# Kernel optimization log

Hardware: AMD Instinct MI355X
Metric: run time of the kernel (lower is better)

## Reference

```python
import jax, jax.numpy as jnp
import numpy as np

N = 50000       # n_points
E = 1000000     # number of events
P = 200000      # node_pair_samples
S = 50          # riemann_samples
EPS = 1e-6      # torch PairwiseDistance eps added to the difference
NON_EVENT_W = 1.0


def setup_inputs() -> dict:
    key = jax.random.key(0)
    ks = jax.random.split(key, 8)
    unif = lambda k, shp: (jax.random.uniform(k, shp) * 0.05 - 0.025).astype(jnp.float32)
    return {
        "beta": jnp.full((1, 1), 1.0, dtype=jnp.float32),
        "z0": unif(ks[0], (N, 2)),
        "v0": unif(ks[1], (N, 2)),
        "a0": unif(ks[2], (N, 2)),
        "events_t": (jax.random.uniform(ks[3], (E,)) * 10.0).astype(jnp.float32),
        "events_uv": jax.random.randint(ks[4], (E, 2), 0, N, dtype=jnp.int32),
        "pairs_u": jax.random.randint(ks[5], (P,), 0, N, dtype=jnp.int32),
        "pairs_v": jax.random.randint(ks[6], (P,), 0, N, dtype=jnp.int32),
        "t0": 0,
        "tn": 10,
    }


def reference(beta, z0, v0, a0, events_t, events_uv, pairs_u, pairs_v, t0, tn):
    # ---- event intensity: sum_e (beta - ||z_u(t_e) - z_v(t_e)||) ----
    u = events_uv[:, 0]
    v = events_uv[:, 1]
    t = events_t[:, None]                          # (E,1)
    # z(t) = z0 + v0*t + 0.5*a0*t^2; only the pair difference is needed
    diff = (z0[u] - z0[v]) + (v0[u] - v0[v]) * t + 0.5 * (a0[u] - a0[v]) * t * t + EPS  # (E,2)
    d = jnp.sqrt(jnp.sum(diff * diff, axis=-1))    # (E,)
    n_events = jnp.asarray(d.shape[0], dtype=beta.dtype)
    event_intensity = n_events * beta - jnp.sum(d)  # (1,1)

    # ---- non-event intensity: Riemann midpoint sum of exp(beta - dist) ----
    t0f = jnp.asarray(t0, dtype=jnp.float32)
    tnf = jnp.asarray(tn, dtype=jnp.float32)
    dx = (tnf - t0f) / S
    t_mid = t0f + (jnp.arange(S, dtype=jnp.float32) + 0.5) * dx  # (S,) midpoints of linspace
    dz = (z0[pairs_u] - z0[pairs_v])[:, None, :]   # (P,1,2)
    dv = (v0[pairs_u] - v0[pairs_v])[:, None, :]
    da = (a0[pairs_u] - a0[pairs_v])[:, None, :]
    tm = t_mid[None, :, None]                      # (1,S,1)
    diffp = dz + dv * tm + 0.5 * da * tm * tm + EPS  # (P,S,2)
    dp = jnp.sqrt(jnp.sum(diffp * diffp, axis=-1))   # (P,S)
    non_event_intensity = jnp.sum(jnp.exp(beta[0, 0] - dp)) * dx

    return event_intensity - NON_EVENT_W * non_event_intensity  # (1,1)
```

## Files before the change

### kernel.cpp

```cpp
#include <hip/hip_runtime.h>
#include <hip/hip_fp16.h>

#define N_NODES 50000
#define E_COUNT 1000000
#define HALF_E  (E_COUNT / 2)
#define P_COUNT 200000
#define S_COUNT 50
#define EPS_F   1e-6f

constexpr int TPB = 256;
constexpr int EVENT_BLOCKS = (HALF_E + TPB - 1) / TPB;
constexpr int PAIR_BLOCKS  = (P_COUNT + TPB - 1) / TPB;
constexpr int TOTAL_BLOCKS = EVENT_BLOCKS + PAIR_BLOCKS;

__device__ __forceinline__ float block_reduce_sum(float v) {
    #pragma unroll
    for (int m = 32; m >= 1; m >>= 1) v += __shfl_xor(v, m, 64);
    __shared__ float smem[TPB / 64];
    const int lane = threadIdx.x & 63;
    const int wid  = threadIdx.x >> 6;
    if (lane == 0) smem[wid] = v;
    __syncthreads();
    float r = 0.0f;
    if (threadIdx.x == 0) {
        #pragma unroll
        for (int w = 0; w < TPB / 64; ++w) r += smem[w];
    }
    __syncthreads();
    return r;
}

__global__ __launch_bounds__(TPB) void pack_nodes_kernel(
    const float2* __restrict__ z0,
    const float2* __restrict__ v0,
    const float2* __restrict__ a0,
    float4*       __restrict__ packed)
{
    const int i = blockIdx.x * TPB + threadIdx.x;
    if (i < N_NODES) {
        const float2 z = z0[i], v = v0[i], a = a0[i];
        float4 r;
        r.x = z.x;
        r.y = z.y;
        r.z = __builtin_bit_cast(float, __floats2half2_rn(v.x, v.y));
        r.w = __builtin_bit_cast(float, __floats2half2_rn(a.x, a.y));
        packed[i] = r;
    }
}

__device__ __forceinline__ float event_dist(const float4 pu, const float4 pv,
                                            const float t) {
    const float2 vu = __half22float2(__builtin_bit_cast(__half2, pu.z));
    const float2 vv = __half22float2(__builtin_bit_cast(__half2, pv.z));
    const float2 au = __half22float2(__builtin_bit_cast(__half2, pu.w));
    const float2 av = __half22float2(__builtin_bit_cast(__half2, pv.w));
    const float ht2 = 0.5f * t * t;
    const float fx = (pu.x - pv.x) + (vu.x - vv.x) * t + (au.x - av.x) * ht2 + EPS_F;
    const float fy = (pu.y - pv.y) + (vu.y - vv.y) * t + (au.y - av.y) * ht2 + EPS_F;
    return sqrtf(fx * fx + fy * fy);
}

__global__ __launch_bounds__(TPB) void fused_partials_kernel(
    const float4* __restrict__ packed,
    const float*  __restrict__ events_t,
    const int*    __restrict__ events_uv_flat,
    const int*    __restrict__ pairs_u,
    const int*    __restrict__ pairs_v,
    const int*    __restrict__ t0p,
    const int*    __restrict__ tnp,
    float*        __restrict__ partials)
{
    float acc = 0.0f;
    const int b = blockIdx.x;

    if (b < PAIR_BLOCKS) {
        const int i = b * TPB + threadIdx.x;
        if (i < P_COUNT) {
            const float t0f = (float)t0p[0];
            const float tnf = (float)tnp[0];
            const float dxs = (tnf - t0f) / (float)S_COUNT;
            const int u = __builtin_nontemporal_load(pairs_u + i);
            const int v = __builtin_nontemporal_load(pairs_v + i);
            const float4 pu = packed[u];
            const float4 pv = packed[v];
            const float2 vu = __half22float2(__builtin_bit_cast(__half2, pu.z));
            const float2 vv = __half22float2(__builtin_bit_cast(__half2, pv.z));
            const float2 au = __half22float2(__builtin_bit_cast(__half2, pu.w));
            const float2 av = __half22float2(__builtin_bit_cast(__half2, pv.w));
            const float dzx = pu.x - pv.x,          dzy = pu.y - pv.y;
            const float dvx = vu.x - vv.x,          dvy = vu.y - vv.y;
            const float dax = 0.5f * (au.x - av.x), day = 0.5f * (au.y - av.y);
            float sacc = 0.0f;
            #pragma unroll 5
            for (int s = 0; s < S_COUNT; ++s) {
                const float tm = t0f + ((float)s + 0.5f) * dxs;
                const float fx = dzx + dvx * tm + dax * tm * tm + EPS_F;
                const float fy = dzy + dvy * tm + day * tm * tm + EPS_F;
                const float dp = sqrtf(fx * fx + fy * fy);
                sacc += __expf(-dp);
            }
            acc = sacc;
        }
    } else {
        const int gid = (b - PAIR_BLOCKS) * TPB + threadIdx.x;
        if (gid < HALF_E) {
            const float t0 = __builtin_nontemporal_load(events_t + gid);
            const float t1 = __builtin_nontemporal_load(events_t + gid + HALF_E);
            const int u0 = __builtin_nontemporal_load(events_uv_flat + 2 * gid);
            const int w0 = __builtin_nontemporal_load(events_uv_flat + 2 * gid + 1);
            const int u1 = __builtin_nontemporal_load(events_uv_flat + 2 * (gid + HALF_E));
            const int w1 = __builtin_nontemporal_load(events_uv_flat + 2 * (gid + HALF_E) + 1);
            const float4 p0u = packed[u0];
            const float4 p0v = packed[w0];
            const float4 p1u = packed[u1];
            const float4 p1v = packed[w1];
            acc = event_dist(p0u, p0v, t0) + event_dist(p1u, p1v, t1);
        }
    }

    const float r = block_reduce_sum(acc);
    if (threadIdx.x == 0) partials[b] = r;
}

__global__ __launch_bounds__(TPB) void finalize_kernel(
    const float* __restrict__ partials,
    const float* __restrict__ beta,
    const int*   __restrict__ t0p,
    const int*   __restrict__ tnp,
    float*       __restrict__ out)
{
    float accP = 0.0f, accE = 0.0f;
    for (int i = threadIdx.x; i < PAIR_BLOCKS; i += TPB) accP += partials[i];
    for (int i = PAIR_BLOCKS + threadIdx.x; i < TOTAL_BLOCKS; i += TPB) accE += partials[i];

    const float sumExp = block_reduce_sum(accP);
    const float sumD   = block_reduce_sum(accE);

    if (threadIdx.x == 0) {
        const float bta = beta[0];
        const float t0f = (float)t0p[0];
        const float tnf = (float)tnp[0];
        const float dxs = (tnf - t0f) / (float)S_COUNT;
        const float event_intensity     = (float)E_COUNT * bta - sumD;
        const float non_event_intensity = expf(bta) * sumExp * dxs;
        out[0] = event_intensity - non_event_intensity;
    }
}

extern "C" void kernel_launch(void* const* d_in, const int* in_sizes, int n_in,
                              void* d_out, int out_size, void* d_ws, size_t ws_size,
                              hipStream_t stream) {
    const float*  beta      = (const float*)d_in[0];
    const float2* z0        = (const float2*)d_in[1];
    const float2* v0        = (const float2*)d_in[2];
    const float2* a0        = (const float2*)d_in[3];
    const float*  events_t  = (const float*)d_in[4];
    const int*    events_uv = (const int*)d_in[5];
    const int*    pairs_u   = (const int*)d_in[6];
    const int*    pairs_v   = (const int*)d_in[7];
    const int*    t0p       = (const int*)d_in[8];
    const int*    tnp       = (const int*)d_in[9];

    const size_t packed_off = 16384;
    float* partials = (float*)d_ws;
    float4* packed  = (float4*)((char*)d_ws + packed_off);
    float* out      = (float*)d_out;

    pack_nodes_kernel<<<(N_NODES + TPB - 1) / TPB, TPB, 0, stream>>>(z0, v0, a0, packed);

    fused_partials_kernel<<<TOTAL_BLOCKS, TPB, 0, stream>>>(
        packed, events_t, events_uv, pairs_u, pairs_v, t0p, tnp, partials);

    finalize_kernel<<<1, TPB, 0, stream>>>(partials, beta, t0p, tnp, out);
}
```

Baseline: 28.44 us.

## Fuse final reduction into main kernel via last-block atomic counter; 4 events per thread

```diff
diff --git a/kernel.cpp b/kernel.cpp
--- a/kernel.cpp
+++ b/kernel.cpp
@@ -3,15 +3,16 @@
 
 #define N_NODES 50000
 #define E_COUNT 1000000
-#define HALF_E  (E_COUNT / 2)
 #define P_COUNT 200000
 #define S_COUNT 50
 #define EPS_F   1e-6f
 
 constexpr int TPB = 256;
-constexpr int EVENT_BLOCKS = (HALF_E + TPB - 1) / TPB;
+constexpr int EPT = 4;
+constexpr int EQ  = E_COUNT / EPT;
+constexpr int EVENT_BLOCKS = (EQ + TPB - 1) / TPB;
 constexpr int PAIR_BLOCKS  = (P_COUNT + TPB - 1) / TPB;
-constexpr int TOTAL_BLOCKS = EVENT_BLOCKS + PAIR_BLOCKS;
+constexpr int TOTAL_BLOCKS = PAIR_BLOCKS + EVENT_BLOCKS;
 
 __device__ __forceinline__ float block_reduce_sum(float v) {
     #pragma unroll
@@ -34,9 +35,11 @@
     const float2* __restrict__ z0,
     const float2* __restrict__ v0,
     const float2* __restrict__ a0,
-    float4*       __restrict__ packed)
+    float4*       __restrict__ packed,
+    unsigned*     __restrict__ counter)
 {
     const int i = blockIdx.x * TPB + threadIdx.x;
+    if (i == 0) *counter = 0u;
     if (i < N_NODES) {
         const float2 z = z0[i], v = v0[i], a = a0[i];
         float4 r;
@@ -60,15 +63,18 @@
     return sqrtf(fx * fx + fy * fy);
 }
 
-__global__ __launch_bounds__(TPB) void fused_partials_kernel(
+__global__ __launch_bounds__(TPB) void fused_kernel(
     const float4* __restrict__ packed,
     const float*  __restrict__ events_t,
     const int*    __restrict__ events_uv_flat,
     const int*    __restrict__ pairs_u,
     const int*    __restrict__ pairs_v,
+    const float*  __restrict__ beta,
     const int*    __restrict__ t0p,
     const int*    __restrict__ tnp,
-    float*        __restrict__ partials)
+    float*        __restrict__ partials,
+    unsigned*     __restrict__ counter,
+    float*        __restrict__ out)
 {
     float acc = 0.0f;
     const int b = blockIdx.x;
@@ -103,47 +109,61 @@
         }
     } else {
         const int gid = (b - PAIR_BLOCKS) * TPB + threadIdx.x;
-        if (gid < HALF_E) {
-            const float t0 = __builtin_nontemporal_load(events_t + gid);
-            const float t1 = __builtin_nontemporal_load(events_t + gid + HALF_E);
-            const int u0 = __builtin_nontemporal_load(events_uv_flat + 2 * gid);
-            const int w0 = __builtin_nontemporal_load(events_uv_flat + 2 * gid + 1);
-            const int u1 = __builtin_nontemporal_load(events_uv_flat + 2 * (gid + HALF_E));
-            const int w1 = __builtin_nontemporal_load(events_uv_flat + 2 * (gid + HALF_E) + 1);
-            const float4 p0u = packed[u0];
-            const float4 p0v = packed[w0];
-            const float4 p1u = packed[u1];
-            const float4 p1v = packed[w1];
-            acc = event_dist(p0u, p0v, t0) + event_dist(p1u, p1v, t1);
+        if (gid < EQ) {
+            float t[EPT];
+            int   iu[EPT], iv[EPT];
+            #pragma unroll
+            for (int k = 0; k < EPT; ++k) {
+                const int e = gid + k * EQ;
+                t[k]  = __builtin_nontemporal_load(events_t + e);
+                iu[k] = __builtin_nontemporal_load(events_uv_flat + 2 * e);
+                iv[k] = __builtin_nontemporal_load(events_uv_flat + 2 * e + 1);
+            }
+            float4 pu[EPT], pv[EPT];
+            #pragma unroll
+            for (int k = 0; k < EPT; ++k) {
+                pu[k] = packed[iu[k]];
+                pv[k] = packed[iv[k]];
+            }
+            float s = 0.0f;
+            #pragma unroll
+            for (int k = 0; k < EPT; ++k) s += event_dist(pu[k], pv[k], t[k]);
+            acc = s;
         }
     }
 
     const float r = block_reduce_sum(acc);
-    if (threadIdx.x == 0) partials[b] = r;
-}
 
-__global__ __launch_bounds__(TPB) void finalize_kernel(
-    const float* __restrict__ partials,
-    const float* __restrict__ beta,
-    const int*   __restrict__ t0p,
-    const int*   __restrict__ tnp,
-    float*       __restrict__ out)
-{
-    float accP = 0.0f, accE = 0.0f;
-    for (int i = threadIdx.x; i < PAIR_BLOCKS; i += TPB) accP += partials[i];
-    for (int i = PAIR_BLOCKS + threadIdx.x; i < TOTAL_BLOCKS; i += TPB) accE += partials[i];
+    __shared__ bool is_last;
+    if (threadIdx.x == 0) {
+        __hip_atomic_store(&partials[b], r, __ATOMIC_RELEASE, __HIP_MEMORY_SCOPE_AGENT);
+        const unsigned old = __hip_atomic_fetch_add(counter, 1u, __ATOMIC_ACQ_REL,
+                                                    __HIP_MEMORY_SCOPE_AGENT);
+        is_last = (old == (unsigned)(TOTAL_BLOCKS - 1));
+    }
+    __syncthreads();
 
-    const float sumExp = block_reduce_sum(accP);
-    const float sumD   = block_reduce_sum(accE);
+    if (is_last) {
+        float accP = 0.0f, accE = 0.0f;
+        for (int i = threadIdx.x; i < PAIR_BLOCKS; i += TPB)
+            accP += __hip_atomic_load(&partials[i], __ATOMIC_ACQUIRE,
+                                      __HIP_MEMORY_SCOPE_AGENT);
+        for (int i = PAIR_BLOCKS + threadIdx.x; i < TOTAL_BLOCKS; i += TPB)
+            accE += __hip_atomic_load(&partials[i], __ATOMIC_ACQUIRE,
+                                      __HIP_MEMORY_SCOPE_AGENT);
 
-    if (threadIdx.x == 0) {
-        const float bta = beta[0];
-        const float t0f = (float)t0p[0];
-        const float tnf = (float)tnp[0];
-        const float dxs = (tnf - t0f) / (float)S_COUNT;
-        const float event_intensity     = (float)E_COUNT * bta - sumD;
-        const float non_event_intensity = expf(bta) * sumExp * dxs;
-        out[0] = event_intensity - non_event_intensity;
+        const float sumExp = block_reduce_sum(accP);
+        const float sumD   = block_reduce_sum(accE);
+
+        if (threadIdx.x == 0) {
+            const float bta = beta[0];
+            const float t0f = (float)t0p[0];
+            const float tnf = (float)tnp[0];
+            const float dxs = (tnf - t0f) / (float)S_COUNT;
+            const float event_intensity     = (float)E_COUNT * bta - sumD;
+            const float non_event_intensity = expf(bta) * sumExp * dxs;
+            out[0] = event_intensity - non_event_intensity;
+        }
     }
 }
 
@@ -161,15 +181,15 @@
     const int*    t0p       = (const int*)d_in[8];
     const int*    tnp       = (const int*)d_in[9];
 
-    const size_t packed_off = 16384;
-    float* partials = (float*)d_ws;
-    float4* packed  = (float4*)((char*)d_ws + packed_off);
-    float* out      = (float*)d_out;
+    float*    partials = (float*)d_ws;
+    unsigned* counter  = (unsigned*)((char*)d_ws + 8192);
+    float4*   packed   = (float4*)((char*)d_ws + 16384);
+    float*    out      = (float*)d_out;
 
-    pack_nodes_kernel<<<(N_NODES + TPB - 1) / TPB, TPB, 0, stream>>>(z0, v0, a0, packed);
+    pack_nodes_kernel<<<(N_NODES + TPB - 1) / TPB, TPB, 0, stream>>>(
+        z0, v0, a0, packed, counter);
 
-    fused_partials_kernel<<<TOTAL_BLOCKS, TPB, 0, stream>>>(
-        packed, events_t, events_uv, pairs_u, pairs_v, t0p, tnp, partials);
-
-    finalize_kernel<<<1, TPB, 0, stream>>>(partials, beta, t0p, tnp, out);
+    fused_kernel<<<TOTAL_BLOCKS, TPB, 0, stream>>>(
+        packed, events_t, events_uv, pairs_u, pairs_v,
+        beta, t0p, tnp, partials, counter, out);
 }
```

Result: slower. 71.16 us (+150.2%).
